# Kernel tuning notes

Hardware: AMD Instinct MI355X
Metric: run time of the kernel (lower is better)

Reference implementation:

```python
import jax, jax.numpy as jnp
import numpy as np

CANVAS = 28      # canvas_size
P = 2            # num_paths
S = 3            # num_segments
PPP = S * 3 + 1  # points_per_path = 10
T = 32           # samples per bezier segment
SS = 2           # 2x2 = 4 supersamples per pixel (num_samples=4)
MARGIN = 2.0
TAU = 0.5        # anti-alias softness of coverage (differentiable rasterizer)
LATENT = 64
HIDDEN = 512


def _leaky(x):
    return jnp.where(x >= 0, x, 0.2 * x)


def _encoder(x, e_w1, e_b1, e_w2, e_b2, w_mu, b_mu, w_lv, b_lv):
    h = x.reshape(x.shape[0], -1)
    h = _leaky(h @ e_w1 + e_b1)
    h = _leaky(h @ e_w2 + e_b2)
    return h @ w_mu + b_mu, h @ w_lv + b_lv


def _decoder(z, d_w1, d_b1, d_w2, d_b2, p_w, p_b, wd_w, wd_b, a_w, a_b):
    B = z.shape[0]
    h = jax.nn.selu(z @ d_w1 + d_b1)
    h = jax.nn.selu(h @ d_w2 + d_b2)
    pts = jnp.tanh(h @ p_w + p_b).reshape(B, P, PPP, 2)
    pts = pts * (CANVAS / 2 - MARGIN) + CANVAS / 2
    # stack overlapping cubic segments: [B,P,S,4,2]
    cp = jnp.stack([pts[:, :, 3 * s:3 * s + 4, :] for s in range(S)], axis=2)
    widths = jax.nn.sigmoid(h @ wd_w + wd_b) * 2.0 + 1.0  # [B,P]
    alphas = jax.nn.sigmoid(h @ a_w + a_b)                # [B,P]
    return cp, widths, alphas


def _render(cp, widths, alphas):
    """Differentiable supersampled stroke rasterizer, white bg, 1-x flip."""
    B = cp.shape[0]
    t = (jnp.arange(T, dtype=cp.dtype) + 0.5) / T
    basis = jnp.stack([(1 - t) ** 3, 3 * t * (1 - t) ** 2,
                       3 * t ** 2 * (1 - t), t ** 3], axis=-1)  # [T,4]
    curve = jnp.einsum('tk,bpskc->bpstc', basis, cp).reshape(B, P, S * T, 2)
    # supersampled pixel sample positions (pixel units)
    coords = (jnp.arange(CANVAS * SS, dtype=cp.dtype) + 0.5) / SS
    ys, xs = jnp.meshgrid(coords, coords, indexing='ij')
    samp = jnp.stack([xs, ys], -1).reshape(-1, 2)  # [N,2], N = (28*2)^2
    # [B,P,N,M] squared distances -> min over curve samples
    d2 = jnp.sum((samp[None, None, :, None, :] - curve[:, :, None, :, :]) ** 2, -1)
    d = jnp.sqrt(jnp.min(d2, axis=-1) + 1e-12)  # [B,P,N]
    cov = jax.nn.sigmoid((widths[..., None] * 0.5 - d) / TAU)
    a = alphas[..., None] * cov                 # per-path ink opacity
    val = jnp.prod(1.0 - a, axis=1)             # composite black ink over bg=1.0
    img = val.reshape(B, CANVAS, SS, CANVAS, SS).mean(axis=(2, 4))
    return 1.0 - img[:, None]                   # [B,1,H,W]


def setup_inputs() -> dict:
    key = jax.random.key(0)
    ks = jax.random.split(key, 24)
    n = lambda k, s, sc=0.05: (jax.random.normal(k, s, dtype=jnp.float32) * sc)
    B = 128
    return {
        'x': jax.random.uniform(ks[0], (B, 1, 28, 28), dtype=jnp.float32),
        'eps': jax.random.normal(ks[1], (B, LATENT), dtype=jnp.float32),
        'e_w1': n(ks[2], (784, 256)), 'e_b1': jnp.zeros(256),
        'e_w2': n(ks[3], (256, 256)), 'e_b2': jnp.zeros(256),
        'w_mu': n(ks[4], (256, LATENT)), 'b_mu': jnp.zeros(LATENT),
        'w_lv': n(ks[5], (256, LATENT)), 'b_lv': jnp.zeros(LATENT),
        'd_w1': n(ks[6], (LATENT, HIDDEN)), 'd_b1': jnp.zeros(HIDDEN),
        'd_w2': n(ks[7], (HIDDEN, HIDDEN)), 'd_b2': jnp.zeros(HIDDEN),
        'p_w': n(ks[8], (HIDDEN, P * PPP * 2)), 'p_b': jnp.zeros(P * PPP * 2),
        'wd_w': n(ks[9], (HIDDEN, P)), 'wd_b': jnp.zeros(P),
        'a_w': n(ks[10], (HIDDEN, P)), 'a_b': jnp.zeros(P),
    }


def reference(x, eps, e_w1, e_b1, e_w2, e_b2, w_mu, b_mu, w_lv, b_lv,
              d_w1, d_b1, d_w2, d_b2, p_w, p_b, wd_w, wd_b, a_w, a_b):
    mu, logvar = _encoder(x, e_w1, e_b1, e_w2, e_b2, w_mu, b_mu, w_lv, b_lv)
    z = mu + eps * jnp.exp(0.5 * logvar)
    cp, widths, alphas = _decoder(z, d_w1, d_b1, d_w2, d_b2,
                                  p_w, p_b, wd_w, wd_b, a_w, a_b)
    rendered = _render(cp, widths, alphas)
    return rendered, mu, logvar, cp, widths, alphas
```

## Files before the change

### kernel.cpp

```cpp
#include <hip/hip_runtime.h>
#include <hip/hip_bf16.h>
#include <math.h>

#define REND_OFF 0
#define MU_OFF   100352
#define LV_OFF   108544
#define CP_OFF   116736
#define W_OFF    122880
#define A_OFF    123136

#define WS_W1 0
#define WS_W2 200704
#define WS_ML 266240
#define WS_D1 299008
#define WS_D2 331776
#define WS_H  593920
#define WS_TOT 626688

__device__ __forceinline__ float leakyf(float x) {
    return x >= 0.f ? x : 0.2f * x;
}
__device__ __forceinline__ float seluf(float x) {
    const float sc = 1.0507009873554805f;
    const float al = 1.6732632423543772f;
    return x > 0.f ? sc * x : sc * al * expm1f(x);
}
__device__ __forceinline__ float sigmoidf(float x) {
    return 1.f / (1.f + expf(-x));
}
__device__ __forceinline__ void bf2(unsigned u, float& lo, float& hi) {
    lo = __uint_as_float(u << 16);
    hi = __uint_as_float(u & 0xffff0000u);
}

__global__ __launch_bounds__(256) void conv_w(
    const float* __restrict__ e_w1, const float* __restrict__ e_w2,
    const float* __restrict__ w_mu, const float* __restrict__ w_lv,
    const float* __restrict__ d_w1, const float* __restrict__ d_w2,
    const float* __restrict__ p_w,  const float* __restrict__ wd_w,
    const float* __restrict__ a_w,  __hip_bfloat16* __restrict__ ws)
{
    int i = blockIdx.x * 256 + threadIdx.x;
    if (i >= WS_TOT) return;
    float v;
    if (i < WS_W2) v = e_w1[i];
    else if (i < WS_ML) v = e_w2[i - WS_W2];
    else if (i < WS_D1) {
        int r = i - WS_ML, k = r >> 7, u = r & 127;
        v = (u < 64) ? w_mu[k * 64 + u] : w_lv[k * 64 + u - 64];
    }
    else if (i < WS_D2) v = d_w1[i - WS_D1];
    else if (i < WS_H)  v = d_w2[i - WS_D2];
    else {
        int r = i - WS_H, k = r >> 6, u = r & 63;
        v = (u < 40) ? p_w[k * 40 + u]
          : (u < 42) ? wd_w[k * 2 + u - 40]
          : (u < 44) ? a_w[k * 2 + u - 42] : 0.f;
    }
    ws[i] = (__hip_bfloat16)v;
}

__global__ __launch_bounds__(1024) void vae_mlp(
    const float* __restrict__ x,    const float* __restrict__ eps,
    const float* __restrict__ e_b1, const float* __restrict__ e_b2,
    const float* __restrict__ b_mu, const float* __restrict__ b_lv,
    const float* __restrict__ d_b1, const float* __restrict__ d_b2,
    const float* __restrict__ p_b,  const float* __restrict__ wd_b,
    const float* __restrict__ a_b,
    const __hip_bfloat16* __restrict__ ws, float* __restrict__ out)
{
    const int b0  = blockIdx.x * 2;
    const int tid = threadIdx.x;

    __shared__ float xs[784 * 2];
    __shared__ float h1[256 * 2];
    __shared__ float h2[256 * 2];
    __shared__ float zs[64 * 2];
    __shared__ float hd1[512 * 2];
    __shared__ float hd2[512 * 2];
    __shared__ float mulv[2][128];
    __shared__ float pts[2][40];
    __shared__ float red[8704];

    for (int i = tid; i < 1568; i += 1024) {
        int bb = i / 784, k = i - bb * 784;
        xs[k * 2 + bb] = x[b0 * 784 + i];
    }
    __syncthreads();

    {
        int jg = tid & 63, ks = tid >> 6;
        const uint2* p = (const uint2*)(ws + WS_W1) + (ks * 49) * 64 + jg;
        const float* xp = xs + (ks * 49) * 2;
        float a0=0,a1=0,a2=0,a3=0,a4=0,a5=0,a6=0,a7=0;
        #pragma unroll 7
        for (int kk = 0; kk < 49; ++kk, p += 64) {
            uint2 w = *p;
            float w0,w1,w2,w3; bf2(w.x,w0,w1); bf2(w.y,w2,w3);
            float x0 = xp[2*kk], x1 = xp[2*kk+1];
            a0 = fmaf(x0,w0,a0); a1 = fmaf(x0,w1,a1);
            a2 = fmaf(x0,w2,a2); a3 = fmaf(x0,w3,a3);
            a4 = fmaf(x1,w0,a4); a5 = fmaf(x1,w1,a5);
            a6 = fmaf(x1,w2,a6); a7 = fmaf(x1,w3,a7);
        }
        float4* r0 = (float4*)&red[(0*16 + ks)*260 + 4*jg];
        float4* r1 = (float4*)&red[(1*16 + ks)*260 + 4*jg];
        *r0 = make_float4(a0,a1,a2,a3);
        *r1 = make_float4(a4,a5,a6,a7);
    }
    __syncthreads();
    if (tid < 512) {
        int b = tid >> 8, j = tid & 255;
        float s = e_b1[j];
        #pragma unroll
        for (int si = 0; si < 16; ++si) s += red[(b*16+si)*260 + j];
        h1[j*2 + b] = leakyf(s);
    }
    __syncthreads();

    {
        int jg = tid & 63, ks = tid >> 6;
        const uint2* p = (const uint2*)(ws + WS_W2) + (ks * 16) * 64 + jg;
        const float* xp = h1 + (ks * 16) * 2;
        float a0=0,a1=0,a2=0,a3=0,a4=0,a5=0,a6=0,a7=0;
        #pragma unroll
        for (int kk = 0; kk < 16; ++kk, p += 64) {
            uint2 w = *p;
            float w0,w1,w2,w3; bf2(w.x,w0,w1); bf2(w.y,w2,w3);
            float x0 = xp[2*kk], x1 = xp[2*kk+1];
            a0 = fmaf(x0,w0,a0); a1 = fmaf(x0,w1,a1);
            a2 = fmaf(x0,w2,a2); a3 = fmaf(x0,w3,a3);
            a4 = fmaf(x1,w0,a4); a5 = fmaf(x1,w1,a5);
            a6 = fmaf(x1,w2,a6); a7 = fmaf(x1,w3,a7);
        }
        float4* r0 = (float4*)&red[(0*16 + ks)*260 + 4*jg];
        float4* r1 = (float4*)&red[(1*16 + ks)*260 + 4*jg];
        *r0 = make_float4(a0,a1,a2,a3);
        *r1 = make_float4(a4,a5,a6,a7);
    }
    __syncthreads();
    if (tid < 512) {
        int b = tid >> 8, j = tid & 255;
        float s = e_b2[j];
        #pragma unroll
        for (int si = 0; si < 16; ++si) s += red[(b*16+si)*260 + j];
        h2[j*2 + b] = leakyf(s);
    }
    __syncthreads();

    {
        int jg = tid & 31, ks = tid >> 5;
        const uint2* p = (const uint2*)(ws + WS_ML) + (ks * 8) * 32 + jg;
        const float* xp = h2 + (ks * 8) * 2;
        float a0=0,a1=0,a2=0,a3=0,a4=0,a5=0,a6=0,a7=0;
        #pragma unroll
        for (int kk = 0; kk < 8; ++kk, p += 32) {
            uint2 w = *p;
            float w0,w1,w2,w3; bf2(w.x,w0,w1); bf2(w.y,w2,w3);
            float x0 = xp[2*kk], x1 = xp[2*kk+1];
            a0 = fmaf(x0,w0,a0); a1 = fmaf(x0,w1,a1);
            a2 = fmaf(x0,w2,a2); a3 = fmaf(x0,w3,a3);
            a4 = fmaf(x1,w0,a4); a5 = fmaf(x1,w1,a5);
            a6 = fmaf(x1,w2,a6); a7 = fmaf(x1,w3,a7);
        }
        float4* r0 = (float4*)&red[(0*32 + ks)*132 + 4*jg];
        float4* r1 = (float4*)&red[(1*32 + ks)*132 + 4*jg];
        *r0 = make_float4(a0,a1,a2,a3);
        *r1 = make_float4(a4,a5,a6,a7);
    }
    __syncthreads();
    if (tid < 256) {
        int b = tid >> 7, u = tid & 127;
        float s = (u < 64) ? b_mu[u] : b_lv[u - 64];
        #pragma unroll
        for (int si = 0; si < 32; ++si) s += red[(b*32+si)*132 + u];
        mulv[b][u] = s;
        int j = u & 63;
        out[(u < 64 ? MU_OFF : LV_OFF) + (b0 + b) * 64 + j] = s;
    }
    __syncthreads();
    if (tid < 128) {
        int b = tid >> 6, j = tid & 63;
        zs[j*2 + b] = fmaf(eps[(b0 + b) * 64 + j], expf(0.5f * mulv[b][64 + j]),
                           mulv[b][j]);
    }
    __syncthreads();

    {
        int jg = tid & 127, ks = tid >> 7;
        const uint2* p = (const uint2*)(ws + WS_D1) + (ks * 8) * 128 + jg;
        const float* xp = zs + (ks * 8) * 2;
        float a0=0,a1=0,a2=0,a3=0,a4=0,a5=0,a6=0,a7=0;
        #pragma unroll
        for (int kk = 0; kk < 8; ++kk, p += 128) {
            uint2 w = *p;
            float w0,w1,w2,w3; bf2(w.x,w0,w1); bf2(w.y,w2,w3);
            float x0 = xp[2*kk], x1 = xp[2*kk+1];
            a0 = fmaf(x0,w0,a0); a1 = fmaf(x0,w1,a1);
            a2 = fmaf(x0,w2,a2); a3 = fmaf(x0,w3,a3);
            a4 = fmaf(x1,w0,a4); a5 = fmaf(x1,w1,a5);
            a6 = fmaf(x1,w2,a6); a7 = fmaf(x1,w3,a7);
        }
        float4* r0 = (float4*)&red[(0*8 + ks)*516 + 4*jg];
        float4* r1 = (float4*)&red[(1*8 + ks)*516 + 4*jg];
        *r0 = make_float4(a0,a1,a2,a3);
        *r1 = make_float4(a4,a5,a6,a7);
    }
    __syncthreads();
    {
        int b = tid >> 9, j = tid & 511;
        float s = d_b1[j];
        #pragma unroll
        for (int si = 0; si < 8; ++si) s += red[(b*8+si)*516 + j];
        hd1[j*2 + b] = seluf(s);
    }
    __syncthreads();

    {
        int jg = tid & 127, ks = tid >> 7;
        const uint2* p = (const uint2*)(ws + WS_D2) + (ks * 64) * 128 + jg;
        const float* xp = hd1 + (ks * 64) * 2;
        float a0=0,a1=0,a2=0,a3=0,a4=0,a5=0,a6=0,a7=0;
        #pragma unroll 8
        for (int kk = 0; kk < 64; ++kk, p += 128) {
            uint2 w = *p;
            float w0,w1,w2,w3; bf2(w.x,w0,w1); bf2(w.y,w2,w3);
            float x0 = xp[2*kk], x1 = xp[2*kk+1];
            a0 = fmaf(x0,w0,a0); a1 = fmaf(x0,w1,a1);
            a2 = fmaf(x0,w2,a2); a3 = fmaf(x0,w3,a3);
            a4 = fmaf(x1,w0,a4); a5 = fmaf(x1,w1,a5);
            a6 = fmaf(x1,w2,a6); a7 = fmaf(x1,w3,a7);
        }
        float4* r0 = (float4*)&red[(0*8 + ks)*516 + 4*jg];
        float4* r1 = (float4*)&red[(1*8 + ks)*516 + 4*jg];
        *r0 = make_float4(a0,a1,a2,a3);
        *r1 = make_float4(a4,a5,a6,a7);
    }
    __syncthreads();
    {
        int b = tid >> 9, j = tid & 511;
        float s = d_b2[j];
        #pragma unroll
        for (int si = 0; si < 8; ++si) s += red[(b*8+si)*516 + j];
        hd2[j*2 + b] = seluf(s);
    }
    __syncthreads();

    {
        int jg = tid & 15, ks = tid >> 4;
        const uint2* p = (const uint2*)(ws + WS_H) + (ks * 8) * 16 + jg;
        const float* xp = hd2 + (ks * 8) * 2;
        float a0=0,a1=0,a2=0,a3=0,a4=0,a5=0,a6=0,a7=0;
        #pragma unroll
        for (int kk = 0; kk < 8; ++kk, p += 16) {
            uint2 w = *p;
            float w0,w1,w2,w3; bf2(w.x,w0,w1); bf2(w.y,w2,w3);
            float x0 = xp[2*kk], x1 = xp[2*kk+1];
            a0 = fmaf(x0,w0,a0); a1 = fmaf(x0,w1,a1);
            a2 = fmaf(x0,w2,a2); a3 = fmaf(x0,w3,a3);
            a4 = fmaf(x1,w0,a4); a5 = fmaf(x1,w1,a5);
            a6 = fmaf(x1,w2,a6); a7 = fmaf(x1,w3,a7);
        }
        float4* r0 = (float4*)&red[(0*64 + ks)*68 + 4*jg];
        float4* r1 = (float4*)&red[(1*64 + ks)*68 + 4*jg];
        *r0 = make_float4(a0,a1,a2,a3);
        *r1 = make_float4(a4,a5,a6,a7);
    }
    __syncthreads();
    if (tid < 128) {
        int b = tid >> 6, u = tid & 63;
        if (u < 44) {
            float s = 0.f;
            #pragma unroll
            for (int si = 0; si < 64; ++si) s += red[(b*64+si)*68 + u];
            if (u < 40) {
                pts[b][u] = tanhf(s + p_b[u]) * 12.f + 14.f;
            } else if (u < 42) {
                out[W_OFF + (b0 + b) * 2 + (u - 40)] =
                    sigmoidf(s + wd_b[u - 40]) * 2.f + 1.f;
            } else {
                out[A_OFF + (b0 + b) * 2 + (u - 42)] = sigmoidf(s + a_b[u - 42]);
            }
        }
    }
    __syncthreads();

    if (tid < 96) {
        int bs = tid / 48, i = tid % 48;
        int p = i / 24, rem = i % 24;
        int s = rem / 8, kc = rem % 8;
        int k = kc >> 1, c = kc & 1;
        out[CP_OFF + (b0 + bs) * 48 + i] = pts[bs][p * 20 + (3 * s + k) * 2 + c];
    }
}

__global__ __launch_bounds__(256) void vae_render(float* __restrict__ out)
{
    const int b   = blockIdx.x;
    const int q   = blockIdx.y;
    const int tid = threadIdx.x;

    __shared__ float2 cur[192];
    __shared__ float  wa[4];

    if (tid < 192) {
        int p = tid / 96;
        int m = tid % 96;
        int s = m / 32;
        int t = m % 32;
        float u  = (t + 0.5f) * (1.f / 32.f);
        float v  = 1.f - u;
        float b0 = v * v * v;
        float b1 = 3.f * u * v * v;
        float b2 = 3.f * u * u * v;
        float b3 = u * u * u;
        const float* cp = out + CP_OFF + b * 48 + p * 24 + s * 8;
        float cx = b0 * cp[0] + b1 * cp[2] + b2 * cp[4] + b3 * cp[6];
        float cy = b0 * cp[1] + b1 * cp[3] + b2 * cp[5] + b3 * cp[7];
        cur[tid] = make_float2(cx, cy);
    } else if (tid < 196) {
        int i = tid - 192;
        wa[i] = (i < 2) ? 0.5f * out[W_OFF + b * 2 + i]
                        : out[A_OFF + b * 2 + (i - 2)];
    }
    __syncthreads();

    if (tid < 196) {
        int Y = tid / 28, X = tid - Y * 28;
        float px0 = X + 0.25f;
        float py0 = (7 * q + Y) + 0.25f;

        float mA[4] = {1e30f, 1e30f, 1e30f, 1e30f};
        float mB[4] = {1e30f, 1e30f, 1e30f, 1e30f};
        #pragma unroll 4
        for (int m = 0; m < 96; ++m) {
            float2 c = cur[m];
            float dx0 = px0 - c.x, dy0 = py0 - c.y;
            float dx1 = dx0 + 0.5f, dy1 = dy0 + 0.5f;
            float xx0 = dx0 * dx0, xx1 = dx1 * dx1;
            float yy0 = dy0 * dy0, yy1 = dy1 * dy1;
            mA[0] = fminf(mA[0], xx0 + yy0);
            mA[1] = fminf(mA[1], xx1 + yy0);
            mA[2] = fminf(mA[2], xx0 + yy1);
            mA[3] = fminf(mA[3], xx1 + yy1);
        }
        #pragma unroll 4
        for (int m = 96; m < 192; ++m) {
            float2 c = cur[m];
            float dx0 = px0 - c.x, dy0 = py0 - c.y;
            float dx1 = dx0 + 0.5f, dy1 = dy0 + 0.5f;
            float xx0 = dx0 * dx0, xx1 = dx1 * dx1;
            float yy0 = dy0 * dy0, yy1 = dy1 * dy1;
            mB[0] = fminf(mB[0], xx0 + yy0);
            mB[1] = fminf(mB[1], xx1 + yy0);
            mB[2] = fminf(mB[2], xx0 + yy1);
            mB[3] = fminf(mB[3], xx1 + yy1);
        }

        const float w0 = wa[0], w1 = wa[1], a0 = wa[2], a1 = wa[3];
        float v = 0.f;
        #pragma unroll
        for (int s = 0; s < 4; ++s) {
            float d0 = sqrtf(mA[s] + 1e-12f);
            float d1 = sqrtf(mB[s] + 1e-12f);
            float c0 = a0 / (1.f + expf(-2.f * (w0 - d0)));
            float c1 = a1 / (1.f + expf(-2.f * (w1 - d1)));
            v += (1.f - c0) * (1.f - c1);
        }
        out[REND_OFF + b * 784 + (7 * q + Y) * 28 + X] = 1.f - 0.25f * v;
    }
}

extern "C" void kernel_launch(void* const* d_in, const int* in_sizes, int n_in,
                              void* d_out, int out_size, void* d_ws, size_t ws_size,
                              hipStream_t stream) {
    const float* x    = (const float*)d_in[0];
    const float* eps  = (const float*)d_in[1];
    const float* e_w1 = (const float*)d_in[2];
    const float* e_b1 = (const float*)d_in[3];
    const float* e_w2 = (const float*)d_in[4];
    const float* e_b2 = (const float*)d_in[5];
    const float* w_mu = (const float*)d_in[6];
    const float* b_mu = (const float*)d_in[7];
    const float* w_lv = (const float*)d_in[8];
    const float* b_lv = (const float*)d_in[9];
    const float* d_w1 = (const float*)d_in[10];
    const float* d_b1 = (const float*)d_in[11];
    const float* d_w2 = (const float*)d_in[12];
    const float* d_b2 = (const float*)d_in[13];
    const float* p_w  = (const float*)d_in[14];
    const float* p_b  = (const float*)d_in[15];
    const float* wd_w = (const float*)d_in[16];
    const float* wd_b = (const float*)d_in[17];
    const float* a_w  = (const float*)d_in[18];
    const float* a_b  = (const float*)d_in[19];
    float* out = (float*)d_out;
    __hip_bfloat16* ws = (__hip_bfloat16*)d_ws;

    hipLaunchKernelGGL(conv_w, dim3(2448), dim3(256), 0, stream,
                       e_w1, e_w2, w_mu, w_lv, d_w1, d_w2, p_w, wd_w, a_w, ws);
    hipLaunchKernelGGL(vae_mlp, dim3(64), dim3(1024), 0, stream,
                       x, eps, e_b1, e_b2, b_mu, b_lv, d_b1, d_b2,
                       p_b, wd_b, a_b, ws, out);
    hipLaunchKernelGGL(vae_render, dim3(128, 4), dim3(256), 0, stream, out);
}
```

Before: 134.4 us.

## Split fused MLP kernel into per-layer column-tiled GEMM launches

Replaces the single 64-block fused MLP kernel, where each block handles two batch rows through all layers, with six separate kernel launches. Each layer is a GEMM tiled over both output columns and batch groups of four rows, with intermediate activations kept in workspace. The aim is to spread weight reads across many more blocks and reuse each weight load across four batch rows. The cost is extra launch overhead, global round trips for intermediate activations, and dependencies between launches.

```diff
diff --git a/kernel.cpp b/kernel.cpp
--- a/kernel.cpp
+++ b/kernel.cpp
@@ -16,6 +16,12 @@
 #define WS_D2 331776
 #define WS_H  593920
 #define WS_TOT 626688
+
+#define AF_H1 0
+#define AF_H2 32768
+#define AF_Z  65536
+#define AF_D1 73728
+#define AF_D2 139264
 
 __device__ __forceinline__ float leakyf(float x) {
     return x >= 0.f ? x : 0.2f * x;
@@ -60,219 +66,185 @@
     ws[i] = (__hip_bfloat16)v;
 }
 
-__global__ __launch_bounds__(1024) void vae_mlp(
-    const float* __restrict__ x,    const float* __restrict__ eps,
-    const float* __restrict__ e_b1, const float* __restrict__ e_b2,
+template<int K, int N, int NT, int ACT>
+__global__ __launch_bounds__(256) void gemm_act(
+    const float* __restrict__ A, const __hip_bfloat16* __restrict__ Wb,
+    const float* __restrict__ bias, float* __restrict__ C)
+{
+    constexpr int BT  = 4;
+    constexpr int JG  = NT / 4;
+    constexpr int S   = 256 / JG;
+    constexpr int Ks  = K / S;
+    constexpr int NTp = NT + 4;
+    static_assert(BT * NT == 256, "epilogue mapping");
+    static_assert(S * Ks == K, "k split");
+
+    const int tid = threadIdx.x;
+    const int b0  = blockIdx.y * BT;
+    const int nb  = blockIdx.x;
+
+    __shared__ __align__(16) float Atile[BT * K];
+    __shared__ __align__(16) float red[BT * S * NTp];
+
+    for (int i = tid; i < BT * K; i += 256) {
+        int b = i / K, k = i - b * K;
+        Atile[k * BT + b] = A[(b0 + b) * K + k];
+    }
+    __syncthreads();
+
+    {
+        const int jg = tid % JG, ks = tid / JG;
+        const int col0 = nb * NT + 4 * jg;
+        const uint2* wp = (const uint2*)Wb + (ks * Ks) * (N / 4) + (col0 >> 2);
+        const float4* xp = (const float4*)Atile + ks * Ks;
+        float a00=0,a01=0,a02=0,a03=0, a10=0,a11=0,a12=0,a13=0;
+        float a20=0,a21=0,a22=0,a23=0, a30=0,a31=0,a32=0,a33=0;
+        #pragma unroll 4
+        for (int kk = 0; kk < Ks; ++kk) {
+            uint2 w = wp[kk * (N / 4)];
+            float w0,w1,w2,w3; bf2(w.x,w0,w1); bf2(w.y,w2,w3);
+            float4 xv = xp[kk];
+            a00 = fmaf(xv.x,w0,a00); a01 = fmaf(xv.x,w1,a01);
+            a02 = fmaf(xv.x,w2,a02); a03 = fmaf(xv.x,w3,a03);
+            a10 = fmaf(xv.y,w0,a10); a11 = fmaf(xv.y,w1,a11);
+            a12 = fmaf(xv.y,w2,a12); a13 = fmaf(xv.y,w3,a13);
+            a20 = fmaf(xv.z,w0,a20); a21 = fmaf(xv.z,w1,a21);
+            a22 = fmaf(xv.z,w2,a22); a23 = fmaf(xv.z,w3,a23);
+            a30 = fmaf(xv.w,w0,a30); a31 = fmaf(xv.w,w1,a31);
+            a32 = fmaf(xv.w,w2,a32); a33 = fmaf(xv.w,w3,a33);
+        }
+        *(float4*)&red[(0 * S + ks) * NTp + 4 * jg] = make_float4(a00,a01,a02,a03);
+        *(float4*)&red[(1 * S + ks) * NTp + 4 * jg] = make_float4(a10,a11,a12,a13);
+        *(float4*)&red[(2 * S + ks) * NTp + 4 * jg] = make_float4(a20,a21,a22,a23);
+        *(float4*)&red[(3 * S + ks) * NTp + 4 * jg] = make_float4(a30,a31,a32,a33);
+    }
+    __syncthreads();
+
+    {
+        int b = tid / NT, j = tid % NT;
+        float s = bias[nb * NT + j];
+        #pragma unroll
+        for (int si = 0; si < S; ++si) s += red[(b * S + si) * NTp + j];
+        s = (ACT == 1) ? leakyf(s) : seluf(s);
+        C[(b0 + b) * N + nb * NT + j] = s;
+    }
+}
+
+__global__ __launch_bounds__(256) void gemm_ml(
+    const float* __restrict__ A, const __hip_bfloat16* __restrict__ Wb,
     const float* __restrict__ b_mu, const float* __restrict__ b_lv,
-    const float* __restrict__ d_b1, const float* __restrict__ d_b2,
-    const float* __restrict__ p_b,  const float* __restrict__ wd_b,
-    const float* __restrict__ a_b,
-    const __hip_bfloat16* __restrict__ ws, float* __restrict__ out)
-{
-    const int b0  = blockIdx.x * 2;
+    const float* __restrict__ eps, float* __restrict__ out,
+    float* __restrict__ Z)
+{
+    constexpr int K = 256, N = 128, JG = 32, S = 8, Ks = 32, NTp = 132, BT = 4;
     const int tid = threadIdx.x;
-
-    __shared__ float xs[784 * 2];
-    __shared__ float h1[256 * 2];
-    __shared__ float h2[256 * 2];
-    __shared__ float zs[64 * 2];
-    __shared__ float hd1[512 * 2];
-    __shared__ float hd2[512 * 2];
-    __shared__ float mulv[2][128];
-    __shared__ float pts[2][40];
-    __shared__ float red[8704];
-
-    for (int i = tid; i < 1568; i += 1024) {
-        int bb = i / 784, k = i - bb * 784;
-        xs[k * 2 + bb] = x[b0 * 784 + i];
-    }
-    __syncthreads();
-
-    {
-        int jg = tid & 63, ks = tid >> 6;
-        const uint2* p = (const uint2*)(ws + WS_W1) + (ks * 49) * 64 + jg;
-        const float* xp = xs + (ks * 49) * 2;
-        float a0=0,a1=0,a2=0,a3=0,a4=0,a5=0,a6=0,a7=0;
-        #pragma unroll 7
-        for (int kk = 0; kk < 49; ++kk, p += 64) {
-            uint2 w = *p;
+    const int b0  = blockIdx.x * BT;
+
+    __shared__ __align__(16) float Atile[BT * K];
+    __shared__ __align__(16) float red[BT * S * NTp];
+    __shared__ float ml[BT][128];
+
+    for (int i = tid; i < BT * K; i += 256) {
+        int b = i / K, k = i - b * K;
+        Atile[k * BT + b] = A[(b0 + b) * K + k];
+    }
+    __syncthreads();
+
+    {
+        const int jg = tid % JG, ks = tid / JG;
+        const uint2* wp = (const uint2*)Wb + (ks * Ks) * (N / 4) + jg;
+        const float4* xp = (const float4*)Atile + ks * Ks;
+        float a00=0,a01=0,a02=0,a03=0, a10=0,a11=0,a12=0,a13=0;
+        float a20=0,a21=0,a22=0,a23=0, a30=0,a31=0,a32=0,a33=0;
+        #pragma unroll 4
+        for (int kk = 0; kk < Ks; ++kk) {
+            uint2 w = wp[kk * (N / 4)];
             float w0,w1,w2,w3; bf2(w.x,w0,w1); bf2(w.y,w2,w3);
-            float x0 = xp[2*kk], x1 = xp[2*kk+1];
-            a0 = fmaf(x0,w0,a0); a1 = fmaf(x0,w1,a1);
-            a2 = fmaf(x0,w2,a2); a3 = fmaf(x0,w3,a3);
-            a4 = fmaf(x1,w0,a4); a5 = fmaf(x1,w1,a5);
-            a6 = fmaf(x1,w2,a6); a7 = fmaf(x1,w3,a7);
-        }
-        float4* r0 = (float4*)&red[(0*16 + ks)*260 + 4*jg];
-        float4* r1 = (float4*)&red[(1*16 + ks)*260 + 4*jg];
-        *r0 = make_float4(a0,a1,a2,a3);
-        *r1 = make_float4(a4,a5,a6,a7);
-    }
-    __syncthreads();
-    if (tid < 512) {
-        int b = tid >> 8, j = tid & 255;
-        float s = e_b1[j];
-        #pragma unroll
-        for (int si = 0; si < 16; ++si) s += red[(b*16+si)*260 + j];
-        h1[j*2 + b] = leakyf(s);
-    }
-    __syncthreads();
-
-    {
-        int jg = tid & 63, ks = tid >> 6;
-        const uint2* p = (const uint2*)(ws + WS_W2) + (ks * 16) * 64 + jg;
-        const float* xp = h1 + (ks * 16) * 2;
-        float a0=0,a1=0,a2=0,a3=0,a4=0,a5=0,a6=0,a7=0;
-        #pragma unroll
-        for (int kk = 0; kk < 16; ++kk, p += 64) {
-            uint2 w = *p;
-            float w0,w1,w2,w3; bf2(w.x,w0,w1); bf2(w.y,w2,w3);
-            float x0 = xp[2*kk], x1 = xp[2*kk+1];
-            a0 = fmaf(x0,w0,a0); a1 = fmaf(x0,w1,a1);
-            a2 = fmaf(x0,w2,a2); a3 = fmaf(x0,w3,a3);
-            a4 = fmaf(x1,w0,a4); a5 = fmaf(x1,w1,a5);
-            a6 = fmaf(x1,w2,a6); a7 = fmaf(x1,w3,a7);
-        }
-        float4* r0 = (float4*)&red[(0*16 + ks)*260 + 4*jg];
-        float4* r1 = (float4*)&red[(1*16 + ks)*260 + 4*jg];
-        *r0 = make_float4(a0,a1,a2,a3);
-        *r1 = make_float4(a4,a5,a6,a7);
-    }
-    __syncthreads();
-    if (tid < 512) {
-        int b = tid >> 8, j = tid & 255;
-        float s = e_b2[j];
-        #pragma unroll
-        for (int si = 0; si < 16; ++si) s += red[(b*16+si)*260 + j];
-        h2[j*2 + b] = leakyf(s);
-    }
-    __syncthreads();
-
-    {
-        int jg = tid & 31, ks = tid >> 5;
-        const uint2* p = (const uint2*)(ws + WS_ML) + (ks * 8) * 32 + jg;
-        const float* xp = h2 + (ks * 8) * 2;
-        float a0=0,a1=0,a2=0,a3=0,a4=0,a5=0,a6=0,a7=0;
-        #pragma unroll
-        for (int kk = 0; kk < 8; ++kk, p += 32) {
-            uint2 w = *p;
-            float w0,w1,w2,w3; bf2(w.x,w0,w1); bf2(w.y,w2,w3);
-            float x0 = xp[2*kk], x1 = xp[2*kk+1];
-            a0 = fmaf(x0,w0,a0); a1 = fmaf(x0,w1,a1);
-            a2 = fmaf(x0,w2,a2); a3 = fmaf(x0,w3,a3);
-            a4 = fmaf(x1,w0,a4); a5 = fmaf(x1,w1,a5);
-            a6 = fmaf(x1,w2,a6); a7 = fmaf(x1,w3,a7);
-        }
-        float4* r0 = (float4*)&red[(0*32 + ks)*132 + 4*jg];
-        float4* r1 = (float4*)&red[(1*32 + ks)*132 + 4*jg];
-        *r0 = make_float4(a0,a1,a2,a3);
-        *r1 = make_float4(a4,a5,a6,a7);
-    }
-    __syncthreads();
-    if (tid < 256) {
-        int b = tid >> 7, u = tid & 127;
+            float4 xv = xp[kk];
+            a00 = fmaf(xv.x,w0,a00); a01 = fmaf(xv.x,w1,a01);
+            a02 = fmaf(xv.x,w2,a02); a03 = fmaf(xv.x,w3,a03);
+            a10 = fmaf(xv.y,w0,a10); a11 = fmaf(xv.y,w1,a11);
+            a12 = fmaf(xv.y,w2,a12); a13 = fmaf(xv.y,w3,a13);
+            a20 = fmaf(xv.z,w0,a20); a21 = fmaf(xv.z,w1,a21);
+            a22 = fmaf(xv.z,w2,a22); a23 = fmaf(xv.z,w3,a23);
+            a30 = fmaf(xv.w,w0,a30); a31 = fmaf(xv.w,w1,a31);
+            a32 = fmaf(xv.w,w2,a32); a33 = fmaf(xv.w,w3,a33);
+        }
+        *(float4*)&red[(0 * S + ks) * NTp + 4 * jg] = make_float4(a00,a01,a02,a03);
+        *(float4*)&red[(1 * S + ks) * NTp + 4 * jg] = make_float4(a10,a11,a12,a13);
+        *(float4*)&red[(2 * S + ks) * NTp + 4 * jg] = make_float4(a20,a21,a22,a23);
+        *(float4*)&red[(3 * S + ks) * NTp + 4 * jg] = make_float4(a30,a31,a32,a33);
+    }
+    __syncthreads();
+
+    for (int t = tid; t < 512; t += 256) {
+        int b = t >> 7, u = t & 127;
         float s = (u < 64) ? b_mu[u] : b_lv[u - 64];
         #pragma unroll
-        for (int si = 0; si < 32; ++si) s += red[(b*32+si)*132 + u];
-        mulv[b][u] = s;
-        int j = u & 63;
-        out[(u < 64 ? MU_OFF : LV_OFF) + (b0 + b) * 64 + j] = s;
-    }
-    __syncthreads();
-    if (tid < 128) {
+        for (int si = 0; si < S; ++si) s += red[(b * S + si) * NTp + u];
+        ml[b][u] = s;
+        out[(u < 64 ? MU_OFF : LV_OFF) + (b0 + b) * 64 + (u & 63)] = s;
+    }
+    __syncthreads();
+    {
         int b = tid >> 6, j = tid & 63;
-        zs[j*2 + b] = fmaf(eps[(b0 + b) * 64 + j], expf(0.5f * mulv[b][64 + j]),
-                           mulv[b][j]);
-    }
-    __syncthreads();
-
-    {
-        int jg = tid & 127, ks = tid >> 7;
-        const uint2* p = (const uint2*)(ws + WS_D1) + (ks * 8) * 128 + jg;
-        const float* xp = zs + (ks * 8) * 2;
-        float a0=0,a1=0,a2=0,a3=0,a4=0,a5=0,a6=0,a7=0;
-        #pragma unroll
-        for (int kk = 0; kk < 8; ++kk, p += 128) {
-            uint2 w = *p;
+        Z[(b0 + b) * 64 + j] = fmaf(eps[(b0 + b) * 64 + j],
+                                    expf(0.5f * ml[b][64 + j]), ml[b][j]);
+    }
+}
+
+__global__ __launch_bounds__(256) void gemm_heads(
+    const float* __restrict__ A, const __hip_bfloat16* __restrict__ Wb,
+    const float* __restrict__ p_b, const float* __restrict__ wd_b,
+    const float* __restrict__ a_b, float* __restrict__ out)
+{
+    constexpr int K = 512, N = 64, JG = 16, S = 16, Ks = 32, NTp = 68, BT = 4;
+    const int tid = threadIdx.x;
+    const int b0  = blockIdx.x * BT;
+
+    __shared__ __align__(16) float Atile[BT * K];
+    __shared__ __align__(16) float red[BT * S * NTp];
+    __shared__ float pts[BT][40];
+
+    for (int i = tid; i < BT * K; i += 256) {
+        int b = i / K, k = i - b * K;
+        Atile[k * BT + b] = A[(b0 + b) * K + k];
+    }
+    __syncthreads();
+
+    {
+        const int jg = tid % JG, ks = tid / JG;
+        const uint2* wp = (const uint2*)Wb + (ks * Ks) * (N / 4) + jg;
+        const float4* xp = (const float4*)Atile + ks * Ks;
+        float a00=0,a01=0,a02=0,a03=0, a10=0,a11=0,a12=0,a13=0;
+        float a20=0,a21=0,a22=0,a23=0, a30=0,a31=0,a32=0,a33=0;
+        #pragma unroll 4
+        for (int kk = 0; kk < Ks; ++kk) {
+            uint2 w = wp[kk * (N / 4)];
             float w0,w1,w2,w3; bf2(w.x,w0,w1); bf2(w.y,w2,w3);
-            float x0 = xp[2*kk], x1 = xp[2*kk+1];
-            a0 = fmaf(x0,w0,a0); a1 = fmaf(x0,w1,a1);
-            a2 = fmaf(x0,w2,a2); a3 = fmaf(x0,w3,a3);
-            a4 = fmaf(x1,w0,a4); a5 = fmaf(x1,w1,a5);
-            a6 = fmaf(x1,w2,a6); a7 = fmaf(x1,w3,a7);
-        }
-        float4* r0 = (float4*)&red[(0*8 + ks)*516 + 4*jg];
-        float4* r1 = (float4*)&red[(1*8 + ks)*516 + 4*jg];
-        *r0 = make_float4(a0,a1,a2,a3);
-        *r1 = make_float4(a4,a5,a6,a7);
-    }
-    __syncthreads();
-    {
-        int b = tid >> 9, j = tid & 511;
-        float s = d_b1[j];
-        #pragma unroll
-        for (int si = 0; si < 8; ++si) s += red[(b*8+si)*516 + j];
-        hd1[j*2 + b] = seluf(s);
-    }
-    __syncthreads();
-
-    {
-        int jg = tid & 127, ks = tid >> 7;
-        const uint2* p = (const uint2*)(ws + WS_D2) + (ks * 64) * 128 + jg;
-        const float* xp = hd1 + (ks * 64) * 2;
-        float a0=0,a1=0,a2=0,a3=0,a4=0,a5=0,a6=0,a7=0;
-        #pragma unroll 8
-        for (int kk = 0; kk < 64; ++kk, p += 128) {
-            uint2 w = *p;
-            float w0,w1,w2,w3; bf2(w.x,w0,w1); bf2(w.y,w2,w3);
-            float x0 = xp[2*kk], x1 = xp[2*kk+1];
-            a0 = fmaf(x0,w0,a0); a1 = fmaf(x0,w1,a1);
-            a2 = fmaf(x0,w2,a2); a3 = fmaf(x0,w3,a3);
-            a4 = fmaf(x1,w0,a4); a5 = fmaf(x1,w1,a5);
-            a6 = fmaf(x1,w2,a6); a7 = fmaf(x1,w3,a7);
-        }
-        float4* r0 = (float4*)&red[(0*8 + ks)*516 + 4*jg];
-        float4* r1 = (float4*)&red[(1*8 + ks)*516 + 4*jg];
-        *r0 = make_float4(a0,a1,a2,a3);
-        *r1 = make_float4(a4,a5,a6,a7);
-    }
-    __syncthreads();
-    {
-        int b = tid >> 9, j = tid & 511;
-        float s = d_b2[j];
-        #pragma unroll
-        for (int si = 0; si < 8; ++si) s += red[(b*8+si)*516 + j];
-        hd2[j*2 + b] = seluf(s);
-    }
-    __syncthreads();
-
-    {
-        int jg = tid & 15, ks = tid >> 4;
-        const uint2* p = (const uint2*)(ws + WS_H) + (ks * 8) * 16 + jg;
-        const float* xp = hd2 + (ks * 8) * 2;
-        float a0=0,a1=0,a2=0,a3=0,a4=0,a5=0,a6=0,a7=0;
-        #pragma unroll
-        for (int kk = 0; kk < 8; ++kk, p += 16) {
-            uint2 w = *p;
-            float w0,w1,w2,w3; bf2(w.x,w0,w1); bf2(w.y,w2,w3);
-            float x0 = xp[2*kk], x1 = xp[2*kk+1];
-            a0 = fmaf(x0,w0,a0); a1 = fmaf(x0,w1,a1);
-            a2 = fmaf(x0,w2,a2); a3 = fmaf(x0,w3,a3);
-            a4 = fmaf(x1,w0,a4); a5 = fmaf(x1,w1,a5);
-            a6 = fmaf(x1,w2,a6); a7 = fmaf(x1,w3,a7);
-        }
-        float4* r0 = (float4*)&red[(0*64 + ks)*68 + 4*jg];
-        float4* r1 = (float4*)&red[(1*64 + ks)*68 + 4*jg];
-        *r0 = make_float4(a0,a1,a2,a3);
-        *r1 = make_float4(a4,a5,a6,a7);
-    }
-    __syncthreads();
-    if (tid < 128) {
+            float4 xv = xp[kk];
+            a00 = fmaf(xv.x,w0,a00); a01 = fmaf(xv.x,w1,a01);
+            a02 = fmaf(xv.x,w2,a02); a03 = fmaf(xv.x,w3,a03);
+            a10 = fmaf(xv.y,w0,a10); a11 = fmaf(xv.y,w1,a11);
+            a12 = fmaf(xv.y,w2,a12); a13 = fmaf(xv.y,w3,a13);
+            a20 = fmaf(xv.z,w0,a20); a21 = fmaf(xv.z,w1,a21);
+            a22 = fmaf(xv.z,w2,a22); a23 = fmaf(xv.z,w3,a23);
+            a30 = fmaf(xv.w,w0,a30); a31 = fmaf(xv.w,w1,a31);
+            a32 = fmaf(xv.w,w2,a32); a33 = fmaf(xv.w,w3,a33);
+        }
+        *(float4*)&red[(0 * S + ks) * NTp + 4 * jg] = make_float4(a00,a01,a02,a03);
+        *(float4*)&red[(1 * S + ks) * NTp + 4 * jg] = make_float4(a10,a11,a12,a13);
+        *(float4*)&red[(2 * S + ks) * NTp + 4 * jg] = make_float4(a20,a21,a22,a23);
+        *(float4*)&red[(3 * S + ks) * NTp + 4 * jg] = make_float4(a30,a31,a32,a33);
+    }
+    __syncthreads();
+
+    {
         int b = tid >> 6, u = tid & 63;
         if (u < 44) {
             float s = 0.f;
             #pragma unroll
-            for (int si = 0; si < 64; ++si) s += red[(b*64+si)*68 + u];
+            for (int si = 0; si < S; ++si) s += red[(b * S + si) * NTp + u];
             if (u < 40) {
                 pts[b][u] = tanhf(s + p_b[u]) * 12.f + 14.f;
             } else if (u < 42) {
@@ -285,12 +257,12 @@
     }
     __syncthreads();
 
-    if (tid < 96) {
-        int bs = tid / 48, i = tid % 48;
+    if (tid < 192) {
+        int bb = tid / 48, i = tid % 48;
         int p = i / 24, rem = i % 24;
         int s = rem / 8, kc = rem % 8;
         int k = kc >> 1, c = kc & 1;
-        out[CP_OFF + (b0 + bs) * 48 + i] = pts[bs][p * 20 + (3 * s + k) * 2 + c];
+        out[CP_OFF + (b0 + bb) * 48 + i] = pts[bb][p * 20 + (3 * s + k) * 2 + c];
     }
 }
 
@@ -396,11 +368,23 @@
     const float* a_b  = (const float*)d_in[19];
     float* out = (float*)d_out;
     __hip_bfloat16* ws = (__hip_bfloat16*)d_ws;
+    float* wsf = (float*)((char*)d_ws + WS_TOT * 2);
 
     hipLaunchKernelGGL(conv_w, dim3(2448), dim3(256), 0, stream,
                        e_w1, e_w2, w_mu, w_lv, d_w1, d_w2, p_w, wd_w, a_w, ws);
-    hipLaunchKernelGGL(vae_mlp, dim3(64), dim3(1024), 0, stream,
-                       x, eps, e_b1, e_b2, b_mu, b_lv, d_b1, d_b2,
-                       p_b, wd_b, a_b, ws, out);
+
+    hipLaunchKernelGGL((gemm_act<784, 256, 64, 1>), dim3(4, 32), dim3(256), 0,
+                       stream, x, ws + WS_W1, e_b1, wsf + AF_H1);
+    hipLaunchKernelGGL((gemm_act<256, 256, 64, 1>), dim3(4, 32), dim3(256), 0,
+                       stream, wsf + AF_H1, ws + WS_W2, e_b2, wsf + AF_H2);
+    hipLaunchKernelGGL(gemm_ml, dim3(32), dim3(256), 0, stream,
+                       wsf + AF_H2, ws + WS_ML, b_mu, b_lv, eps, out, wsf + AF_Z);
+    hipLaunchKernelGGL((gemm_act<64, 512, 64, 2>), dim3(8, 32), dim3(256), 0,
+                       stream, wsf + AF_Z, ws + WS_D1, d_b1, wsf + AF_D1);
+    hipLaunchKernelGGL((gemm_act<512, 512, 64, 2>), dim3(8, 32), dim3(256), 0,
+                       stream, wsf + AF_D1, ws + WS_D2, d_b2, wsf + AF_D2);
+    hipLaunchKernelGGL(gemm_heads, dim3(32), dim3(256), 0, stream,
+                       wsf + AF_D2, ws + WS_H, p_b, wd_b, a_b, out);
+
     hipLaunchKernelGGL(vae_render, dim3(128, 4), dim3(256), 0, stream, out);
 }
```

New measurement: 149.2 us. 1.11x slower.
